# Kernel tuning notes

Hardware: AMD Instinct MI355X
Metric: run time of the kernel (lower is better)

## Reference

```python
import jax, jax.numpy as jnp
import numpy as np

TOP_K = 2
SMOOTHING = 0.9


def setup_inputs() -> dict:
    key = jax.random.key(0)
    k1, k2, k3 = jax.random.split(key, 3)
    T, D, E = 16384, 2048, 64
    x = jax.random.normal(k1, (T, D), dtype=jnp.float32)
    gate_w = jax.random.normal(k2, (D, E), dtype=jnp.float32) * (1.0 / np.sqrt(D))
    expert_loads = jax.random.uniform(k3, (E,), dtype=jnp.float32)
    expert_loads = expert_loads / jnp.sum(expert_loads)  # normalized load estimate
    return {"x": x, "gate_w": gate_w, "expert_loads": expert_loads}


def reference(x, gate_w, expert_loads):
    T, _ = x.shape
    E = gate_w.shape[1]
    # Gate projection: [T, D] @ [D, E] -> [T, E]
    logits = jnp.matmul(x, gate_w)
    # Load-balancing bias injection (ExpertLoadBalancer.get_balancing_biases):
    # bias = -(load - 1/E) * 2, added to logits for expert *selection* only.
    biases = -(expert_loads - 1.0 / E) * 2.0
    _, top_idx = jax.lax.top_k(logits + biases[None, :], TOP_K)  # [T, K] int32
    # Routing weights: softmax over the selected (unbiased) logits.
    top_logits = jnp.take_along_axis(logits, top_idx, axis=1)  # [T, K]
    routing_weights = jax.nn.softmax(top_logits, axis=-1)  # [T, K]
    # Vectorized load update (replaces the Python double loop in update_loads):
    # scatter-add routing weights per expert, normalize by token count, EMA-smooth.
    current_loads = jax.ops.segment_sum(
        routing_weights.reshape(-1), top_idx.reshape(-1), num_segments=E
    ) / T
    new_loads = SMOOTHING * expert_loads + (1.0 - SMOOTHING) * current_loads
    return routing_weights, top_idx, new_loads
```

## Files before the change

### kernel.cpp

```cpp
#include <hip/hip_runtime.h>

#define TT 16384
#define DD 2048
#define EE 64

typedef __attribute__((ext_vector_type(8))) short bf16x8;
typedef __attribute__((ext_vector_type(8))) unsigned short ushort8;
typedef __attribute__((ext_vector_type(4))) float f32x4;
typedef __attribute__((ext_vector_type(16))) float f32x16;

__device__ __forceinline__ unsigned short bf16_rne(float f) {
    unsigned u = __float_as_uint(f);
    return (unsigned short)((u + 0x7FFFu + ((u >> 16) & 1u)) >> 16);
}
__device__ __forceinline__ float bf16_f32(unsigned short h) {
    return __uint_as_float(((unsigned)h) << 16);
}
__device__ __forceinline__ unsigned cvt_pk(float lo, float hi) {
    unsigned r;
    asm("v_cvt_pk_bf16_f32 %0, %1, %2" : "=v"(r) : "v"(lo), "v"(hi));
    return r;
}
__device__ __forceinline__ bf16x8 pack4(unsigned a, unsigned b, unsigned c, unsigned d) {
    union { unsigned u[4]; bf16x8 v; } t;
    t.u[0] = a; t.u[1] = b; t.u[2] = c; t.u[3] = d;
    return t.v;
}
__device__ __forceinline__ void gload16(void* lds, const void* g) {
    __builtin_amdgcn_global_load_lds(
        (const __attribute__((address_space(1))) unsigned int*)g,
        (__attribute__((address_space(3))) unsigned int*)lds, 16, 0, 0);
}

__global__ __launch_bounds__(256)
void wconv(const float* __restrict__ wg, unsigned short* __restrict__ wpack) {
    const int g = (int)blockIdx.x * 256 + threadIdx.x;
    const int t = g >> 8, m = (g >> 7) & 1, h = (g >> 6) & 1, lane = g & 63;
    const int e = m * 32 + (lane & 31);
    const int ks = t * 16 + (lane >> 5) * 8;
    ushort8 v;
#pragma unroll
    for (int j = 0; j < 8; ++j) {
        const float f = wg[(size_t)(ks + j) * EE + e];
        const unsigned short hi = bf16_rne(f);
        v[j] = h ? bf16_rne(f - bf16_f32(hi)) : hi;
    }
    *(ushort8*)(wpack + (size_t)g * 8) = v;
}

__global__ __launch_bounds__(512, 4)
void gate_fused(const float* __restrict__ x, const unsigned short* __restrict__ wpack,
                const float* __restrict__ loads, float* __restrict__ out,
                float* __restrict__ binpart) {
    __shared__ __align__(16) float arena[16384];
    __shared__ float bins[64];

    const int tid = threadIdx.x, lane = tid & 63, q = tid >> 6;
    const int tb = (int)blockIdx.x;
    const int tok = lane & 31, hi5 = lane >> 5;

    f32x16 acc[2];
#pragma unroll
    for (int m = 0; m < 2; ++m)
#pragma unroll
        for (int r = 0; r < 16; ++r) acc[m][r] = 0.0f;

    auto stage_x = [&](int s, float* rb) {
#pragma unroll
        for (int i = 0; i < 4; ++i) {
            const int row = i * 8 + (lane >> 3);
            const int c = (lane & 7) ^ (lane >> 3);
            gload16(rb + q * 1024 + i * 256,
                    x + (size_t)(tb * 32 + row) * DD + q * 256 + s * 32 + c * 4);
        }
    };
    bf16x8 W[8];
    auto loadW = [&](int s) {
        const unsigned short* base =
            wpack + (size_t)((q * 16 + s * 2) * 4) * 512 + lane * 8;
#pragma unroll
        for (int f = 0; f < 8; ++f)
            W[f] = *(const bf16x8*)(base + (size_t)f * 512);
    };
    auto compute = [&](const float* rb) {
        const float* xq = rb + q * 1024 + tok * 32;
        const int key = tok & 7;
#pragma unroll
        for (int ts = 0; ts < 2; ++ts) {
            const int c0 = ts * 4 + hi5 * 2;
            const f32x4 va = *(const f32x4*)(xq + ((c0) ^ key) * 4);
            const f32x4 vb = *(const f32x4*)(xq + ((c0 + 1) ^ key) * 4);
            const float cf[8] = {va.x, va.y, va.z, va.w, vb.x, vb.y, vb.z, vb.w};
            unsigned ph[4], pl[4];
#pragma unroll
            for (int j = 0; j < 4; ++j) {
                ph[j] = cvt_pk(cf[2 * j], cf[2 * j + 1]);
                const float h0 = __uint_as_float(ph[j] << 16);
                const float h1 = __uint_as_float(ph[j] & 0xFFFF0000u);
                pl[j] = cvt_pk(cf[2 * j] - h0, cf[2 * j + 1] - h1);
            }
            const bf16x8 bhi = pack4(ph[0], ph[1], ph[2], ph[3]);
            const bf16x8 blo = pack4(pl[0], pl[1], pl[2], pl[3]);
#pragma unroll
            for (int m = 0; m < 2; ++m) {
                acc[m] = __builtin_amdgcn_mfma_f32_32x32x16_bf16(
                    W[ts * 4 + m * 2], bhi, acc[m], 0, 0, 0);
                acc[m] = __builtin_amdgcn_mfma_f32_32x32x16_bf16(
                    W[ts * 4 + m * 2], blo, acc[m], 0, 0, 0);
                acc[m] = __builtin_amdgcn_mfma_f32_32x32x16_bf16(
                    W[ts * 4 + m * 2 + 1], bhi, acc[m], 0, 0, 0);
            }
        }
    };

    stage_x(0, arena);
    loadW(0);
    stage_x(1, arena + 8192);
    asm volatile("s_waitcnt vmcnt(12)" ::: "memory");
    __builtin_amdgcn_s_barrier();

#pragma unroll 1
    for (int s = 0; s < 8; ++s) {
        compute((s & 1) ? arena + 8192 : arena);
        __builtin_amdgcn_s_barrier();
        if (s < 6) {
            loadW(s + 1);
            stage_x(s + 2, (s & 1) ? arena + 8192 : arena);
            asm volatile("s_waitcnt vmcnt(12)" ::: "memory");
            __builtin_amdgcn_s_barrier();
        } else if (s == 6) {
            loadW(7);
            asm volatile("s_waitcnt vmcnt(8)" ::: "memory");
            __builtin_amdgcn_s_barrier();
        }
    }

    if (q != 0) {
        float* ov = arena + (size_t)(q - 1) * 2304 + lane * 36;
#pragma unroll
        for (int m = 0; m < 2; ++m)
#pragma unroll
            for (int p = 0; p < 4; ++p) {
                const f32x4 t_ = {acc[m][p * 4], acc[m][p * 4 + 1],
                                  acc[m][p * 4 + 2], acc[m][p * 4 + 3]};
                *(f32x4*)(ov + m * 16 + p * 4) = t_;
            }
    }
    __syncthreads();
    if (q != 0) return;

#pragma unroll 1
    for (int qq = 0; qq < 7; ++qq) {
        const float* ov = arena + (size_t)qq * 2304 + lane * 36;
#pragma unroll
        for (int m = 0; m < 2; ++m)
#pragma unroll
            for (int p = 0; p < 4; ++p) {
                const f32x4 t_ = *(const f32x4*)(ov + m * 16 + p * 4);
#pragma unroll
                for (int j = 0; j < 4; ++j) acc[m][p * 4 + j] += t_[j];
            }
    }

    float v1 = -3.4e38f, u1 = 0.0f, v2 = -3.4e38f, u2 = 0.0f;
    int i1 = 0x7fffffff, i2 = 0x7fffffff;
#pragma unroll
    for (int m = 0; m < 2; ++m)
#pragma unroll
        for (int r = 0; r < 16; ++r) {
            const int e = m * 32 + (r & 3) + 8 * (r >> 2) + 4 * hi5;
            const float u = acc[m][r];
            const float b = u - (loads[e] - 0.015625f) * 2.0f;
            if ((b > v1) || (b == v1 && e < i1)) {
                v2 = v1; u2 = u1; i2 = i1;
                v1 = b;  u1 = u;  i1 = e;
            } else if ((b > v2) || (b == v2 && e < i2)) {
                v2 = b; u2 = u; i2 = e;
            }
        }
    {
        const float ov1 = __shfl_xor(v1, 32), ou1 = __shfl_xor(u1, 32);
        const float ov2 = __shfl_xor(v2, 32), ou2 = __shfl_xor(u2, 32);
        const int oi1 = __shfl_xor(i1, 32), oi2 = __shfl_xor(i2, 32);
        if ((ov1 > v1) || (ov1 == v1 && oi1 < i1)) {
            if ((v1 > ov2) || (v1 == ov2 && i1 < oi2)) { v2 = v1; u2 = u1; i2 = i1; }
            else                                        { v2 = ov2; u2 = ou2; i2 = oi2; }
            v1 = ov1; u1 = ou1; i1 = oi1;
        } else if ((ov1 > v2) || (ov1 == v2 && oi1 < i2)) {
            v2 = ov1; u2 = ou1; i2 = oi1;
        }
    }

    bins[lane] = 0.0f;
    if (lane < 32) {
        const int tg = tb * 32 + tok;
        const float mx = fmaxf(u1, u2);
        const float e1 = __expf(u1 - mx), e2 = __expf(u2 - mx);
        const float w1 = e1 / (e1 + e2), w2 = e2 / (e1 + e2);
        *(float2*)(out + 2 * tg) = make_float2(w1, w2);
        *(float2*)(out + 2 * TT + 2 * tg) = make_float2((float)i1, (float)i2);
        atomicAdd(&bins[i1], w1);
        atomicAdd(&bins[i2], w2);
    }
    binpart[(size_t)tb * 64 + lane] = bins[lane];
}

__global__ __launch_bounds__(256)
void finalize1(const float* __restrict__ binpart, float* __restrict__ binmid) {
    __shared__ float p[4][64];
    const int e = threadIdx.x & 63, sub = threadIdx.x >> 6;
    float s = 0.0f;
#pragma unroll
    for (int r = 0; r < 8; ++r)
        s += binpart[(size_t)(((int)blockIdx.x * 4 + sub) * 8 + r) * 64 + e];
    p[sub][e] = s;
    __syncthreads();
    if (sub == 0)
        binmid[(int)blockIdx.x * 64 + e] = ((p[0][e] + p[1][e]) + p[2][e]) + p[3][e];
}

__global__ __launch_bounds__(64)
void finalize2(const float* __restrict__ binmid, const float* __restrict__ loads,
               float* __restrict__ out) {
    const int e = threadIdx.x;
    float s = 0.0f;
#pragma unroll
    for (int j = 0; j < 16; ++j) s += binmid[j * 64 + e];
    out[4 * TT + e] = 0.9f * loads[e] + 0.1f * (s * (1.0f / 16384.0f));
}

extern "C" void kernel_launch(void* const* d_in, const int* in_sizes, int n_in,
                              void* d_out, int out_size, void* d_ws, size_t ws_size,
                              hipStream_t stream) {
    const float* x = (const float*)d_in[0];
    const float* wg = (const float*)d_in[1];
    const float* loads = (const float*)d_in[2];
    float* out = (float*)d_out;

    unsigned short* wpack = (unsigned short*)d_ws;
    float* binpart = (float*)(wpack + (size_t)64 * 8 * 64 * 8);
    float* binmid = binpart + 512 * 64;

    hipLaunchKernelGGL(wconv, dim3(128), dim3(256), 0, stream, wg, wpack);
    hipLaunchKernelGGL(gate_fused, dim3(512), dim3(512), 0, stream,
                       x, wpack, loads, out, binpart);
    hipLaunchKernelGGL(finalize1, dim3(16), dim3(256), 0, stream, binpart, binmid);
    hipLaunchKernelGGL(finalize2, dim3(1), dim3(64), 0, stream, binmid, loads, out);
}
```

Before: 45.88 us.

## Deepen gate GEMM pipeline to 4-slot per-wave ring and merge finalize kernels

```diff
diff --git a/kernel.cpp b/kernel.cpp
--- a/kernel.cpp
+++ b/kernel.cpp
@@ -65,76 +65,74 @@
 #pragma unroll
         for (int r = 0; r < 16; ++r) acc[m][r] = 0.0f;
 
-    auto stage_x = [&](int s, float* rb) {
-#pragma unroll
-        for (int i = 0; i < 4; ++i) {
-            const int row = i * 8 + (lane >> 3);
-            const int c = (lane & 7) ^ (lane >> 3);
-            gload16(rb + q * 1024 + i * 256,
-                    x + (size_t)(tb * 32 + row) * DD + q * 256 + s * 32 + c * 4);
+    auto slotp = [&](int r) { return arena + r * 4096 + q * 512; };
+
+    auto stage_x = [&](int s, int r) {
+        float* rb = slotp(r);
+#pragma unroll
+        for (int i = 0; i < 2; ++i) {
+            const int row = i * 16 + (lane >> 2);
+            const int c = (lane & 3) ^ ((lane >> 2) & 3) ^ ((i & 1) << 1);
+            gload16(rb + i * 256,
+                    x + (size_t)(tb * 32 + row) * DD + q * 256 + s * 16 + c * 4);
         }
     };
-    bf16x8 W[8];
-    auto loadW = [&](int s) {
+    auto loadW = [&](int s, bf16x8 (&Wr)[4]) {
         const unsigned short* base =
-            wpack + (size_t)((q * 16 + s * 2) * 4) * 512 + lane * 8;
-#pragma unroll
-        for (int f = 0; f < 8; ++f)
-            W[f] = *(const bf16x8*)(base + (size_t)f * 512);
+            wpack + ((size_t)(q * 16 + s) * 4) * 512 + lane * 8;
+#pragma unroll
+        for (int f = 0; f < 4; ++f)
+            Wr[f] = *(const bf16x8*)(base + (size_t)f * 512);
     };
-    auto compute = [&](const float* rb) {
-        const float* xq = rb + q * 1024 + tok * 32;
-        const int key = tok & 7;
-#pragma unroll
-        for (int ts = 0; ts < 2; ++ts) {
-            const int c0 = ts * 4 + hi5 * 2;
-            const f32x4 va = *(const f32x4*)(xq + ((c0) ^ key) * 4);
-            const f32x4 vb = *(const f32x4*)(xq + ((c0 + 1) ^ key) * 4);
-            const float cf[8] = {va.x, va.y, va.z, va.w, vb.x, vb.y, vb.z, vb.w};
-            unsigned ph[4], pl[4];
-#pragma unroll
-            for (int j = 0; j < 4; ++j) {
-                ph[j] = cvt_pk(cf[2 * j], cf[2 * j + 1]);
-                const float h0 = __uint_as_float(ph[j] << 16);
-                const float h1 = __uint_as_float(ph[j] & 0xFFFF0000u);
-                pl[j] = cvt_pk(cf[2 * j] - h0, cf[2 * j + 1] - h1);
-            }
-            const bf16x8 bhi = pack4(ph[0], ph[1], ph[2], ph[3]);
-            const bf16x8 blo = pack4(pl[0], pl[1], pl[2], pl[3]);
-#pragma unroll
-            for (int m = 0; m < 2; ++m) {
-                acc[m] = __builtin_amdgcn_mfma_f32_32x32x16_bf16(
-                    W[ts * 4 + m * 2], bhi, acc[m], 0, 0, 0);
-                acc[m] = __builtin_amdgcn_mfma_f32_32x32x16_bf16(
-                    W[ts * 4 + m * 2], blo, acc[m], 0, 0, 0);
-                acc[m] = __builtin_amdgcn_mfma_f32_32x32x16_bf16(
-                    W[ts * 4 + m * 2 + 1], bhi, acc[m], 0, 0, 0);
-            }
+    auto compute = [&](int r, bf16x8 (&Wr)[4]) {
+        const float* xq = slotp(r);
+        const int i = tok >> 4;
+        const int cx = (tok & 3) ^ ((i & 1) << 1);
+        const int cb = (tok & 15) * 4;
+        const f32x4 va = *(const f32x4*)(xq + i * 256 + (cb + ((hi5 * 2) ^ cx)) * 4);
+        const f32x4 vb = *(const f32x4*)(xq + i * 256 + (cb + ((hi5 * 2 + 1) ^ cx)) * 4);
+        const float cf[8] = {va.x, va.y, va.z, va.w, vb.x, vb.y, vb.z, vb.w};
+        unsigned ph[4], pl[4];
+#pragma unroll
+        for (int j = 0; j < 4; ++j) {
+            ph[j] = cvt_pk(cf[2 * j], cf[2 * j + 1]);
+            const float h0 = __uint_as_float(ph[j] << 16);
+            const float h1 = __uint_as_float(ph[j] & 0xFFFF0000u);
+            pl[j] = cvt_pk(cf[2 * j] - h0, cf[2 * j + 1] - h1);
+        }
+        const bf16x8 bhi = pack4(ph[0], ph[1], ph[2], ph[3]);
+        const bf16x8 blo = pack4(pl[0], pl[1], pl[2], pl[3]);
+#pragma unroll
+        for (int m = 0; m < 2; ++m) {
+            acc[m] = __builtin_amdgcn_mfma_f32_32x32x16_bf16(Wr[m * 2], bhi, acc[m], 0, 0, 0);
+            acc[m] = __builtin_amdgcn_mfma_f32_32x32x16_bf16(Wr[m * 2], blo, acc[m], 0, 0, 0);
+            acc[m] = __builtin_amdgcn_mfma_f32_32x32x16_bf16(Wr[m * 2 + 1], bhi, acc[m], 0, 0, 0);
         }
     };
 
-    stage_x(0, arena);
-    loadW(0);
-    stage_x(1, arena + 8192);
-    asm volatile("s_waitcnt vmcnt(12)" ::: "memory");
-    __builtin_amdgcn_s_barrier();
-
-#pragma unroll 1
-    for (int s = 0; s < 8; ++s) {
-        compute((s & 1) ? arena + 8192 : arena);
-        __builtin_amdgcn_s_barrier();
-        if (s < 6) {
-            loadW(s + 1);
-            stage_x(s + 2, (s & 1) ? arena + 8192 : arena);
-            asm volatile("s_waitcnt vmcnt(12)" ::: "memory");
-            __builtin_amdgcn_s_barrier();
-        } else if (s == 6) {
-            loadW(7);
-            asm volatile("s_waitcnt vmcnt(8)" ::: "memory");
-            __builtin_amdgcn_s_barrier();
-        }
-    }
-
+    bf16x8 Wr[3][4];
+    stage_x(0, 0);
+    loadW(0, Wr[0]);
+    stage_x(1, 1);
+    loadW(1, Wr[1]);
+    stage_x(2, 2);
+
+#pragma unroll
+    for (int s = 0; s < 13; ++s) {
+        loadW(s + 2, Wr[(s + 2) % 3]);
+        stage_x(s + 3, (s + 3) & 3);
+        asm volatile("s_waitcnt vmcnt(12)" ::: "memory");
+        compute(s & 3, Wr[s % 3]);
+    }
+    loadW(15, Wr[0]);
+    asm volatile("s_waitcnt vmcnt(10)" ::: "memory");
+    compute(13 & 3, Wr[1]);
+    asm volatile("s_waitcnt vmcnt(4)" ::: "memory");
+    compute(14 & 3, Wr[2]);
+    asm volatile("s_waitcnt vmcnt(0)" ::: "memory");
+    compute(15 & 3, Wr[0]);
+
+    __syncthreads();
     if (q != 0) {
         float* ov = arena + (size_t)(q - 1) * 2304 + lane * 36;
 #pragma unroll
@@ -206,27 +204,19 @@
 }
 
 __global__ __launch_bounds__(256)
-void finalize1(const float* __restrict__ binpart, float* __restrict__ binmid) {
+void finalize(const float* __restrict__ binpart, const float* __restrict__ loads,
+              float* __restrict__ out) {
     __shared__ float p[4][64];
     const int e = threadIdx.x & 63, sub = threadIdx.x >> 6;
     float s = 0.0f;
-#pragma unroll
-    for (int r = 0; r < 8; ++r)
-        s += binpart[(size_t)(((int)blockIdx.x * 4 + sub) * 8 + r) * 64 + e];
+#pragma unroll 8
+    for (int r = sub; r < 512; r += 4) s += binpart[(size_t)r * 64 + e];
     p[sub][e] = s;
     __syncthreads();
-    if (sub == 0)
-        binmid[(int)blockIdx.x * 64 + e] = ((p[0][e] + p[1][e]) + p[2][e]) + p[3][e];
-}
-
-__global__ __launch_bounds__(64)
-void finalize2(const float* __restrict__ binmid, const float* __restrict__ loads,
-               float* __restrict__ out) {
-    const int e = threadIdx.x;
-    float s = 0.0f;
-#pragma unroll
-    for (int j = 0; j < 16; ++j) s += binmid[j * 64 + e];
-    out[4 * TT + e] = 0.9f * loads[e] + 0.1f * (s * (1.0f / 16384.0f));
+    if (sub == 0) {
+        const float tot = ((p[0][e] + p[1][e]) + p[2][e]) + p[3][e];
+        out[4 * TT + e] = 0.9f * loads[e] + 0.1f * (tot * (1.0f / 16384.0f));
+    }
 }
 
 extern "C" void kernel_launch(void* const* d_in, const int* in_sizes, int n_in,
@@ -239,11 +229,10 @@
 
     unsigned short* wpack = (unsigned short*)d_ws;
     float* binpart = (float*)(wpack + (size_t)64 * 8 * 64 * 8);
-    float* binmid = binpart + 512 * 64;
 
     hipLaunchKernelGGL(wconv, dim3(128), dim3(256), 0, stream, wg, wpack);
     hipLaunchKernelGGL(gate_fused, dim3(512), dim3(512), 0, stream,
                        x, wpack, loads, out, binpart);
-    hipLaunchKernelGGL(finalize1, dim3(16), dim3(256), 0, stream, binpart, binmid);
-    hipLaunchKernelGGL(finalize2, dim3(1), dim3(64), 0, stream, binmid, loads, out);
-}
+    hipLaunchKernelGGL(finalize, dim3(1), dim3(256), 0, stream,
+                       binpart, loads, out);
+}
```

New measurement: 51.19 us. 1.12x slower.
